# Optimization experiments

Measured on AMD Instinct MI355X. Metric: run time of the kernel, lower is better.

The kernel has to match this reference:

```python
import jax, jax.numpy as jnp
import numpy as np

CUTOFF = 10.0


def _forward(query_points, codes, grid_points, eW1, eb1, eW2, eb2, cW, cb, fcW, fcb, nW1, nb1, nW2, nb2, edge_index):
    B, N, _ = query_points.shape
    G = grid_points.shape[0]
    C = codes.shape[-1]
    n_pts = B * N
    num_nodes = n_pts + B * G
    qp = query_points.reshape(-1, 3)
    gc = jnp.broadcast_to(grid_points[None], (B, G, 3)).reshape(-1, 3)
    x = jnp.concatenate([qp, gc], axis=0)                      # [num_nodes, 3]
    h = jnp.concatenate([jnp.zeros((n_pts, C), qp.dtype), codes.reshape(-1, C)], axis=0)
    row, col = edge_index[0], edge_index[1]                    # row = grid (source), col = query (target)
    ones = jnp.ones((edge_index.shape[1],), x.dtype)
    denom = jnp.maximum(jax.ops.segment_sum(ones, col, num_segments=num_nodes), 1.0)[:, None]

    def layer(x, h, We1, be1, We2, be2, Wc, bc, Wn1, bn1, Wn2, bn2, out_x_dim):
        rel = x[row] - x[col]                                  # [E, 3]
        dist = jnp.linalg.norm(rel, axis=-1, keepdims=True)    # [E, 1]
        m = jax.nn.silu(jnp.concatenate([h[row], h[col], dist], axis=-1) @ We1 + be1)
        m = jax.nn.silu(m @ We2 + be2)                         # [E, H]
        d = dist[:, 0]
        Cm = 0.5 * (jnp.cos(d * jnp.pi / CUTOFF) + 1.0) * (d <= CUTOFF)
        m = m * Cm[:, None]
        coef = m @ Wc + bc                                     # [E, out_x_dim]
        dirn = rel / (dist + 1e-8)
        if out_x_dim == 1:
            cmsg = coef * dirn                                 # [E, 3]
            dx = jax.ops.segment_sum(cmsg, col, num_segments=num_nodes) / denom
            x_new = x + dx
        else:
            cmsg = (coef[:, :, None] * dirn[:, None, :]).reshape(coef.shape[0], -1)  # [E, T*3]
            dx = (jax.ops.segment_sum(cmsg, col, num_segments=num_nodes) / denom).reshape(num_nodes, out_x_dim, 3)
            x_new = x[:, None, :] + dx                         # [num_nodes, T, 3]
        m_aggr = jax.ops.segment_sum(m, col, num_segments=num_nodes) / denom
        h_delta = jax.nn.silu(jnp.concatenate([h, m_aggr], axis=-1) @ Wn1 + bn1) @ Wn2 + bn2
        return x_new, h + h_delta

    for i in range(3):
        x, h = layer(x, h, eW1[i], eb1[i], eW2[i], eb2[i], cW[i], cb[i], nW1[i], nb1[i], nW2[i], nb2[i], 1)
    T = fcb.shape[0]
    x_f, _ = layer(x, h, eW1[3], eb1[3], eW2[3], eb2[3], fcW, fcb, nW1[3], nb1[3], nW2[3], nb2[3], T)
    pred = x_f[:n_pts].reshape(B, N, T, 3)
    return pred - query_points.reshape(B, N, 3)[:, :, None, :]


def setup_inputs() -> dict:
    key = jax.random.key(0)
    B, N, Gs, Cd, H, T, deg = 8, 2048, 8, 128, 128, 5, 16
    G = Gs ** 3
    n_pts = B * N
    E = n_pts * deg
    ks = jax.random.split(key, 12)
    c1 = (jnp.arange(Gs, dtype=jnp.float32) - (Gs - 1) / 2.0) * 2.0   # anchor_spacing = 2.0, centered
    gx, gy, gz = jnp.meshgrid(c1, c1, c1, indexing='ij')
    grid_points = jnp.stack([gx, gy, gz], -1).reshape(-1, 3)
    query_points = jax.random.uniform(ks[0], (B, N, 3), minval=-7.0, maxval=7.0)
    codes = jax.random.normal(ks[1], (B, G, Cd), dtype=jnp.float32)
    q = jnp.repeat(jnp.arange(n_pts, dtype=jnp.int32), deg)
    gl = jax.random.randint(ks[2], (E,), 0, G, dtype=jnp.int32)
    row = n_pts + (q // N) * G + gl                                   # grid node (global idx), same batch as query
    edge_index = jnp.stack([row, q], axis=0)
    def lin(k, fi, sh):
        return jax.random.normal(k, sh, dtype=jnp.float32) / jnp.sqrt(jnp.float32(fi))
    eW1 = lin(ks[3], 2 * Cd + 1, (4, 2 * Cd + 1, H)); eb1 = jnp.zeros((4, H))
    eW2 = lin(ks[4], H, (4, H, H)); eb2 = jnp.zeros((4, H))
    cW = lin(ks[5], H, (3, H, 1)); cb = jnp.zeros((3, 1))
    fcW = lin(ks[6], H, (H, T)); fcb = jnp.zeros((T,))
    nW1 = lin(ks[7], Cd + H, (4, Cd + H, H)); nb1 = jnp.zeros((4, H))
    nW2 = lin(ks[8], H, (4, H, Cd)); nb2 = jnp.zeros((4, Cd))
    return {"query_points": query_points, "codes": codes, "grid_points": grid_points,
            "eW1": eW1, "eb1": eb1, "eW2": eW2, "eb2": eb2,
            "cW": cW, "cb": cb, "fcW": fcW, "fcb": fcb,
            "nW1": nW1, "nb1": nb1, "nW2": nW2, "nb2": nb2,
            "edge_index": edge_index}


def reference(query_points, codes, grid_points, eW1, eb1, eW2, eb2, cW, cb, fcW, fcb, nW1, nb1, nW2, nb2, edge_index):
    return _forward(query_points, codes, grid_points, eW1, eb1, eW2, eb2, cW, cb, fcW, fcb, nW1, nb1, nW2, nb2, edge_index)
```

## Files before the change

### kernel.cpp

```cpp
#include <hip/hip_runtime.h>
#include <hip/hip_bf16.h>

typedef unsigned short u16;
typedef unsigned int u32;
typedef __attribute__((ext_vector_type(8))) short short8;
typedef __attribute__((ext_vector_type(4))) float floatx4;

#define N_PTS 16384
#define N_GRID 4096
#define GPTS 512
#define HD 128
#define DEG 16
#define QB 16
#define EB 256
#define EBLK (N_PTS / QB)

__device__ __forceinline__ float silu_f(float x) {
    return x * __builtin_amdgcn_rcpf(1.0f + __expf(-x));
}
__device__ __forceinline__ short f2bf(float x) { return (short)__bfloat16_as_ushort(__float2bfloat16(x)); }

__global__ void k_fillf(float* out, float v, int n) {
    int i = blockIdx.x * blockDim.x + threadIdx.x;
    if (i < n) out[i] = v;
}

__global__ void k_init(const float* __restrict__ qp, const float* __restrict__ codes,
                       float* __restrict__ x_q, float* __restrict__ h_g, float* __restrict__ h_q,
                       float* __restrict__ Bq) {
    int stride = gridDim.x * blockDim.x;
    int i0 = blockIdx.x * blockDim.x + threadIdx.x;
    for (int i = i0; i < N_PTS * 3; i += stride) x_q[i] = qp[i];
    for (int i = i0; i < N_GRID * HD; i += stride) h_g[i] = codes[i];
    for (int i = i0; i < N_PTS * HD; i += stride) { h_q[i] = 0.0f; Bq[i] = 0.0f; }
}

__global__ void k_prep(const float* __restrict__ eW2, short* __restrict__ wsT) {
    int idx = blockIdx.x * blockDim.x + threadIdx.x;
    if (idx >= 4 * HD * HD) return;
    int l = idx >> 14, rem = idx & 16383, f = rem >> 7, k = rem & 127;
    wsT[idx] = f2bf(eW2[l * 16384 + k * HD + f]);
}

__global__ void k_prep2(const float* __restrict__ nW1, const float* __restrict__ nW2,
                        const float* __restrict__ eW1,
                        short* __restrict__ nW1T, short* __restrict__ nW2T,
                        short* __restrict__ W1midT, short* __restrict__ W1topT) {
    int idx = blockIdx.x * blockDim.x + threadIdx.x;
    if (idx < 3 * 32768) {
        int l = idx >> 15, r = idx & 32767, f = r >> 8, k = r & 255;
        nW1T[idx] = f2bf(nW1[l * 32768 + k * 128 + f]);
    } else if (idx < 3 * 32768 + 3 * 16384) {
        int j = idx - 3 * 32768;
        int l = j >> 14, r = j & 16383, f = r >> 7, k = r & 127;
        nW2T[j] = f2bf(nW2[l * 16384 + k * 128 + f]);
    } else if (idx < 3 * 32768 + 6 * 16384) {
        int j = idx - 3 * 32768 - 3 * 16384;
        int p = j >> 14, r = j & 16383, f = r >> 7, k = r & 127;
        W1midT[j] = f2bf(eW1[(p + 1) * 257 * 128 + (128 + k) * 128 + f]);
    } else if (idx < 3 * 32768 + 6 * 16384 + 4 * 16384) {
        int j = idx - 3 * 32768 - 6 * 16384;
        int l = j >> 14, r = j & 16383, f = r >> 7, k = r & 127;
        W1topT[j] = f2bf(eW1[l * 257 * 128 + k * 128 + f]);
    }
}

__device__ __forceinline__ void stageB(short* Bb, const short* src, int rowF4, int colF4, int tid) {
#pragma unroll
    for (int s = 0; s < 8; s++) {
        int idx = s * 256 + tid;
        int f = idx >> 4, c4 = idx & 15;
        float4 v = ((const float4*)src)[f * rowF4 + colF4 + c4];
        *(float4*)((char*)Bb + ((idx * 16) ^ ((f & 7) << 4))) = v;
    }
}

__device__ __forceinline__ void nb_gemm(const short* X1, const short* Bb, floatx4* acc,
                                        int rowbase, int kOff, int quad, int c, int swz) {
#pragma unroll
    for (int ks = 0; ks < 4; ks++) {
        short8 a = *(const short8*)((const char*)X1 + rowbase + (((kOff + ks * 32 + quad * 8) * 2) ^ swz));
#pragma unroll
        for (int n = 0; n < 8; n++) {
            short8 b = *(const short8*)((const char*)Bb + ((((n * 16 + c) << 8) + (ks * 32 + quad * 8) * 2) ^ swz));
            acc[n] = __builtin_amdgcn_mfma_f32_16x16x32_bf16(a, b, acc[n], 0, 0, 0);
        }
    }
}

__global__ __launch_bounds__(256) void k_ga2(
    const float* __restrict__ hg, float* __restrict__ Ag,
    const short* __restrict__ W1topT, const float* __restrict__ b1,
    const short* __restrict__ Wn1T, const float* __restrict__ bn1,
    const short* __restrict__ Wn2T, const float* __restrict__ bn2,
    int updateH, float* __restrict__ hg_out) {
    __shared__ short X[64 * 128];
    __shared__ short Bb[128 * 128];
    int tid = threadIdx.x;
    int n0 = blockIdx.x * 64;
    int wid = tid >> 6, lane = tid & 63, quad = lane >> 4, c = lane & 15;
    const int swz = (c & 7) << 4;

    {
        int q = tid >> 2, part = tid & 3;
        const float* src = &hg[(n0 + q) * HD + part * 32];
        int wswz = (q & 7) << 4;
#pragma unroll
        for (int i = 0; i < 4; i++) {
            float4 a = ((const float4*)src)[2 * i];
            float4 b = ((const float4*)src)[2 * i + 1];
            short8 v;
            v[0] = f2bf(a.x); v[1] = f2bf(a.y); v[2] = f2bf(a.z); v[3] = f2bf(a.w);
            v[4] = f2bf(b.x); v[5] = f2bf(b.y); v[6] = f2bf(b.z); v[7] = f2bf(b.w);
            *(short8*)((char*)X + ((q * 256 + part * 64 + i * 16) ^ wswz)) = v;
        }
    }
    stageB(Bb, W1topT, 16, 0, tid);
    __syncthreads();

    int rowbase = (wid * 16 + c) * 256;
    floatx4 acc[8];
#pragma unroll
    for (int n = 0; n < 8; n++) acc[n] = (floatx4)0.f;
    nb_gemm(X, Bb, acc, rowbase, 0, quad, c, swz);
#pragma unroll
    for (int n = 0; n < 8; n++) {
        int f = n * 16 + c;
        float bv = b1[f];
#pragma unroll
        for (int r = 0; r < 4; r++)
            Ag[(n0 + wid * 16 + quad * 4 + r) * HD + f] = acc[n][r] + bv;
    }
    if (!updateH) return;

    __syncthreads();
    stageB(Bb, Wn1T, 32, 0, tid);
    __syncthreads();
#pragma unroll
    for (int n = 0; n < 8; n++) acc[n] = (floatx4)0.f;
    nb_gemm(X, Bb, acc, rowbase, 0, quad, c, swz);
    __syncthreads();
#pragma unroll
    for (int n = 0; n < 8; n++) {
        int f = n * 16 + c;
        float b1v = bn1[f];
#pragma unroll
        for (int r = 0; r < 4; r++) {
            int rq = wid * 16 + quad * 4 + r;
            *(short*)((char*)X + ((rq * 256 + f * 2) ^ ((rq & 7) << 4))) =
                f2bf(silu_f(acc[n][r] + b1v));
        }
    }
    stageB(Bb, Wn2T, 16, 0, tid);
    __syncthreads();
#pragma unroll
    for (int n = 0; n < 8; n++) acc[n] = (floatx4)0.f;
    nb_gemm(X, Bb, acc, rowbase, 0, quad, c, swz);
#pragma unroll
    for (int n = 0; n < 8; n++) {
        int f = n * 16 + c;
        float b2v2 = bn2[f];
#pragma unroll
        for (int r = 0; r < 4; r++) {
            int gn = n0 + wid * 16 + quad * 4 + r;
            hg_out[gn * HD + f] = hg[gn * HD + f] + acc[n][r] + b2v2;
        }
    }
}

__global__ __launch_bounds__(256) void k_nb2(
    float* __restrict__ hq, const float* __restrict__ mg,
    const float* __restrict__ bn1, const float* __restrict__ bn2,
    const short* __restrict__ W1T, const short* __restrict__ W2T,
    const short* __restrict__ W3T, float* __restrict__ Bq) {
    __shared__ short X1[64 * 256];
    __shared__ short Bb[128 * 128];
    int tid = threadIdx.x;
    int q0 = blockIdx.x * 64;
    int wid = tid >> 6, lane = tid & 63, quad = lane >> 4, c = lane & 15;
    const int swz = (c & 7) << 4;

    {
        int q = tid >> 2, part = tid & 3;
        const float* src = (part < 2) ? &hq[(q0 + q) * HD + (part & 1) * 64]
                                      : &mg[(q0 + q) * HD + (part & 1) * 64];
        int wswz = (q & 7) << 4;
#pragma unroll
        for (int i = 0; i < 8; i++) {
            float4 a = ((const float4*)src)[2 * i];
            float4 b = ((const float4*)src)[2 * i + 1];
            short8 v;
            v[0] = f2bf(a.x); v[1] = f2bf(a.y); v[2] = f2bf(a.z); v[3] = f2bf(a.w);
            v[4] = f2bf(b.x); v[5] = f2bf(b.y); v[6] = f2bf(b.z); v[7] = f2bf(b.w);
            *(short8*)((char*)X1 + ((q * 512 + part * 128 + i * 16) ^ wswz)) = v;
        }
    }
    stageB(Bb, W1T, 32, 0, tid);
    __syncthreads();

    int row = wid * 16 + c;
    int rowbase = row * 512;
    floatx4 acc[8];
#pragma unroll
    for (int n = 0; n < 8; n++) acc[n] = (floatx4)0.f;
    nb_gemm(X1, Bb, acc, rowbase, 0, quad, c, swz);
    __syncthreads();
    stageB(Bb, W1T, 32, 16, tid);
    __syncthreads();
    nb_gemm(X1, Bb, acc, rowbase, 128, quad, c, swz);
    __syncthreads();

#pragma unroll
    for (int n = 0; n < 8; n++) {
        int f = n * 16 + c;
        float b1v = bn1[f];
#pragma unroll
        for (int r = 0; r < 4; r++) {
            int rq = wid * 16 + quad * 4 + r;
            *(short*)((char*)X1 + ((rq * 512 + (128 + f) * 2) ^ ((rq & 7) << 4))) =
                f2bf(silu_f(acc[n][r] + b1v));
        }
    }
    stageB(Bb, W2T, 16, 0, tid);
    __syncthreads();

#pragma unroll
    for (int n = 0; n < 8; n++) acc[n] = (floatx4)0.f;
    nb_gemm(X1, Bb, acc, rowbase, 128, quad, c, swz);
    __syncthreads();

#pragma unroll
    for (int n = 0; n < 8; n++) {
        int f = n * 16 + c;
        float b2v2 = bn2[f];
#pragma unroll
        for (int r = 0; r < 4; r++) {
            int rq = wid * 16 + quad * 4 + r;
            int gq = q0 + rq;
            float hv = hq[gq * HD + f] + acc[n][r] + b2v2;
            hq[gq * HD + f] = hv;
            *(short*)((char*)X1 + ((rq * 512 + f * 2) ^ ((rq & 7) << 4))) = f2bf(hv);
        }
    }
    stageB(Bb, W3T, 16, 0, tid);
    __syncthreads();

#pragma unroll
    for (int n = 0; n < 8; n++) acc[n] = (floatx4)0.f;
    nb_gemm(X1, Bb, acc, rowbase, 0, quad, c, swz);
#pragma unroll
    for (int n = 0; n < 8; n++) {
        int f = n * 16 + c;
#pragma unroll
        for (int r = 0; r < 4; r++) {
            int gq = q0 + wid * 16 + quad * 4 + r;
            Bq[gq * HD + f] = acc[n][r];
        }
    }
}

template <int OUTT, bool FIN>
__global__ __launch_bounds__(512, 4) void k_edge(
    const float* __restrict__ Ag, const float* __restrict__ Bq, float* __restrict__ x_q,
    const float* __restrict__ wdrow, const short* __restrict__ wsT,
    const float* __restrict__ b2v, const float* __restrict__ Wc, const float* __restrict__ cbp,
    const int* __restrict__ erow, const float* __restrict__ gridp,
    const float* __restrict__ qp, float* __restrict__ out, float* __restrict__ maggr) {
    __shared__ float misc[3072];
    __shared__ short lwsT[HD * HD];
    int tid = threadIdx.x;

    float* sdist = misc;
    float* scm   = misc + 256;
    float* sdir  = misc + 512;
    float* xs    = misc + 1280;
    float* scoef = misc + 1344;
    int*   sgi   = (int*)(misc + 2624);

    int q0 = blockIdx.x * QB;
    int wid = tid >> 6, lane = tid & 63, quad = lane >> 4, c = lane & 15;

    if (tid < QB * 3) xs[tid] = x_q[q0 * 3 + tid];
    {
        const float4* src = (const float4*)wsT;
#pragma unroll
        for (int s = 0; s < 4; s++) {
            int idx = s * 512 + tid;
            int byte = idx << 4;
            int swz2 = byte ^ (((byte >> 8) & 7) << 4);
            *(float4*)((char*)lwsT + swz2) = src[idx];
        }
    }
    __syncthreads();
    if (tid < EB) {
        int e = tid, q = e >> 4;
        int gi = erow[q0 * DEG + e] - N_PTS;
        sgi[e] = gi;
        int gl = gi & (GPTS - 1);
        float r0 = gridp[gl * 3 + 0] - xs[q * 3 + 0];
        float r1 = gridp[gl * 3 + 1] - xs[q * 3 + 1];
        float r2 = gridp[gl * 3 + 2] - xs[q * 3 + 2];
        float dist = sqrtf(r0 * r0 + r1 * r1 + r2 * r2);
        float inv = 1.0f / (dist + 1e-8f);
        sdist[e] = dist;
        sdir[0 * EB + e] = r0 * inv;
        sdir[1 * EB + e] = r1 * inv;
        sdir[2 * EB + e] = r2 * inv;
        float cw = 0.5f * (__cosf(dist * 0.31415926535897931f) + 1.0f);
        scm[e] = (dist <= 10.0f) ? cw : 0.0f;
    }
    __syncthreads();

    int gi_[2]; float dist_[2];
#pragma unroll
    for (int mi = 0; mi < 2; mi++) {
        int e = (wid * 2 + mi) * 16 + c;
        gi_[mi] = sgi[e];
        dist_[mi] = sdist[e];
    }

    floatx4 acc[2][8];
#pragma unroll
    for (int mi = 0; mi < 2; mi++)
#pragma unroll
        for (int n = 0; n < 8; n++) acc[mi][n] = (floatx4)0.f;

    const int swz = (c & 7) << 4;

#pragma unroll
    for (int ch = 0; ch < 4; ch++) {
        int kb = ch * 32 + quad * 8;
        float4 wd0 = *(const float4*)(wdrow + kb);
        float4 wd1 = *(const float4*)(wdrow + kb + 4);
        short8 afr[2];
#pragma unroll
        for (int mi = 0; mi < 2; mi++) {
            int q = wid * 2 + mi;
            float dist = dist_[mi];
            const float4* ap = (const float4*)(Ag + gi_[mi] * HD + kb);
            float4 a0 = ap[0], a1 = ap[1];
            const float4* bp4 = (const float4*)(Bq + (q0 + q) * HD + kb);
            float4 b0 = bp4[0], b1 = bp4[1];
            short8 v;
            v[0] = f2bf(silu_f(a0.x + b0.x + dist * wd0.x));
            v[1] = f2bf(silu_f(a0.y + b0.y + dist * wd0.y));
            v[2] = f2bf(silu_f(a0.z + b0.z + dist * wd0.z));
            v[3] = f2bf(silu_f(a0.w + b0.w + dist * wd0.w));
            v[4] = f2bf(silu_f(a1.x + b1.x + dist * wd1.x));
            v[5] = f2bf(silu_f(a1.y + b1.y + dist * wd1.y));
            v[6] = f2bf(silu_f(a1.z + b1.z + dist * wd1.z));
            v[7] = f2bf(silu_f(a1.w + b1.w + dist * wd1.w));
            afr[mi] = v;
        }
#pragma unroll
        for (int n = 0; n < 8; n++) {
            int byte = ((n * 16 + c) << 8) + (kb << 1);
            short8 bfr = *(const short8*)((const char*)lwsT + (byte ^ swz));
            acc[0][n] = __builtin_amdgcn_mfma_f32_16x16x32_bf16(afr[0], bfr, acc[0][n], 0, 0, 0);
            acc[1][n] = __builtin_amdgcn_mfma_f32_16x16x32_bf16(afr[1], bfr, acc[1][n], 0, 0, 0);
        }
    }

#pragma unroll
    for (int mi = 0; mi < 2; mi++) {
        int q = wid * 2 + mi;
        int ebase = q * 16;
        float cmr[4];
#pragma unroll
        for (int r = 0; r < 4; r++) cmr[r] = scm[ebase + quad * 4 + r];
        float apc[4][OUTT];
#pragma unroll
        for (int r = 0; r < 4; r++)
#pragma unroll
            for (int t = 0; t < OUTT; t++) apc[r][t] = 0.f;
#pragma unroll
        for (int n = 0; n < 8; n++) {
            int f = n * 16 + c;
            float be2v = b2v[f];
            float wcv[OUTT];
            if (FIN) {
#pragma unroll
                for (int t = 0; t < OUTT; t++) wcv[t] = Wc[f * 5 + t];
            } else {
                wcv[0] = Wc[f];
            }
            float cs = 0.f;
#pragma unroll
            for (int r = 0; r < 4; r++) {
                float v = silu_f(acc[mi][n][r] + be2v) * cmr[r];
                cs += v;
#pragma unroll
                for (int t = 0; t < OUTT; t++) apc[r][t] += v * wcv[t];
            }
            cs += __shfl_xor(cs, 16, 64);
            cs += __shfl_xor(cs, 32, 64);
            if (!FIN && lane < 16) maggr[(q0 + q) * HD + f] = cs * 0.0625f;
        }
#pragma unroll
        for (int t = 0; t < OUTT; t++) {
#pragma unroll
            for (int r = 0; r < 4; r++) {
                float v = apc[r][t];
                v += __shfl_xor(v, 1, 64);
                v += __shfl_xor(v, 2, 64);
                v += __shfl_xor(v, 4, 64);
                v += __shfl_xor(v, 8, 64);
                if (c == 0) scoef[(ebase + quad * 4 + r) * OUTT + t] = v;
            }
        }
    }
    __syncthreads();

    if (tid < QB * 3 * OUTT) {
        int qq = tid / (3 * OUTT), rem = tid % (3 * OUTT), t = rem / 3, c2 = rem % 3;
        float cbv = cbp[t];
        float s = 0.f;
#pragma unroll 4
        for (int r = 0; r < 16; r++) {
            int ee = qq * 16 + r;
            s += (scoef[ee * OUTT + t] + cbv) * sdir[c2 * EB + ee];
        }
        float dd = s * 0.0625f;
        if (FIN) out[(q0 + qq) * 15 + t * 3 + c2] = xs[qq * 3 + c2] + dd - qp[(q0 + qq) * 3 + c2];
        else x_q[(q0 + qq) * 3 + c2] = xs[qq * 3 + c2] + dd;
    }
}

extern "C" void kernel_launch(void* const* d_in, const int* in_sizes, int n_in,
                              void* d_out, int out_size, void* d_ws, size_t ws_size,
                              hipStream_t stream) {
    float* out = (float*)d_out;
    int fill_blocks = (out_size + 255) / 256;

    static const int exp_sz[16] = { 49152, 524288, 1536, 131584, 512, 65536, 512, 384,
                                    3, 640, 5, 131072, 512, 65536, 512, 524288 };
    bool ok = (n_in == 16);
    for (int i = 0; ok && i < 16; i++) if (in_sizes[i] != exp_sz[i]) ok = false;
    if (!ok || ws_size < (size_t)40 * 1024 * 1024) {
        k_fillf<<<fill_blocks, 256, 0, stream>>>(out, 777.0f, out_size);
        return;
    }

    const float* qp    = (const float*)d_in[0];
    const float* codes = (const float*)d_in[1];
    const float* gridp = (const float*)d_in[2];
    const float* eW1   = (const float*)d_in[3];
    const float* eb1   = (const float*)d_in[4];
    const float* eW2   = (const float*)d_in[5];
    const float* eb2   = (const float*)d_in[6];
    const float* cW    = (const float*)d_in[7];
    const float* cb    = (const float*)d_in[8];
    const float* fcW   = (const float*)d_in[9];
    const float* fcb   = (const float*)d_in[10];
    const float* nW1   = (const float*)d_in[11];
    const float* nb1   = (const float*)d_in[12];
    const float* nW2   = (const float*)d_in[13];
    const float* nb2   = (const float*)d_in[14];
    const int*   erow  = (const int*)d_in[15];

    float* ws = (float*)d_ws;
    float* x_q  = ws;  ws += N_PTS * 3;
    float* h_q  = ws;  ws += N_PTS * HD;
    float* hg_a = ws;  ws += N_GRID * HD;
    float* hg_b = ws;  ws += N_GRID * HD;
    float* Ag0  = ws;  ws += N_GRID * HD;
    float* Ag1  = ws;  ws += N_GRID * HD;
    float* Ag2  = ws;  ws += N_GRID * HD;
    float* Ag3  = ws;  ws += N_GRID * HD;
    float* Bqb  = ws;  ws += N_PTS * HD;
    float* mgb  = ws;  ws += N_PTS * HD;
    short* wsT    = (short*)ws;
    short* nW1T   = wsT + 65536;
    short* nW2T   = nW1T + 98304;
    short* W1midT = nW2T + 49152;
    short* W1topT = W1midT + 49152;
    float* Agb[4] = { Ag0, Ag1, Ag2, Ag3 };
    float* hgs[2] = { hg_a, hg_b };

    k_init<<<2048, 256, 0, stream>>>(qp, codes, x_q, hg_a, h_q, Bqb);
    k_prep<<<(4 * HD * HD + 255) / 256, 256, 0, stream>>>(eW2, wsT);
    k_prep2<<<(3 * 32768 + 6 * 16384 + 4 * 16384 + 255) / 256, 256, 0, stream>>>(
        nW1, nW2, eW1, nW1T, nW2T, W1midT, W1topT);

    for (int L = 0; L < 4; L++) {
        int nl = (L < 3) ? L : 0;
        k_ga2<<<N_GRID / 64, 256, 0, stream>>>(
            hgs[L & 1], Agb[L], W1topT + L * 16384, eb1 + L * 128,
            nW1T + nl * 32768, nb1 + L * 128, nW2T + nl * 16384, nb2 + L * 128,
            (L < 3) ? 1 : 0, hgs[(L + 1) & 1]);
    }

    for (int i = 0; i < 4; i++) {
        int fin = (i == 3);
        const float* W1l = eW1 + i * 257 * 128;
        if (i > 0) {
            int p = i - 1;
            k_nb2<<<N_PTS / 64, 256, 0, stream>>>(h_q, mgb,
                                                  nb1 + p * 128, nb2 + p * 128,
                                                  nW1T + p * 32768, nW2T + p * 16384,
                                                  W1midT + p * 16384, Bqb);
        }
        if (!fin) {
            k_edge<1, false><<<EBLK, 512, 0, stream>>>(
                Agb[i], Bqb, x_q, W1l + 256 * 128, wsT + i * 16384, eb2 + i * 128,
                cW + i * 128, cb + i, erow, gridp, qp, out, mgb);
        } else {
            k_edge<5, true><<<EBLK, 512, 0, stream>>>(
                Agb[3], Bqb, x_q, W1l + 256 * 128, wsT + i * 16384, eb2 + i * 128,
                fcW, fcb, erow, gridp, qp, out, mgb);
        }
    }
}
```

Before: 370.4 us.

## Fuse query node-update MLP into edge kernel epilogue

Removes the separate k_nb2 launch by running the query node-update MLP (h update and the next layer's W1mid projection into Bq) at the end of each k_edge block for its 16 queries. The aggregated messages stay in shared memory as bf16 instead of round-tripping through the global mgb buffer. This saves a global write and read of a 16384x128 float tensor plus three launches. In exchange, each 16-query block restages three 128x128 weight tiles, which is 4x more weight traffic than the old 64-row blocks. Extra shared memory and the lowered launch-bounds occupancy (4 to 3) are also risks.

```diff
diff --git a/kernel.cpp b/kernel.cpp
--- a/kernel.cpp
+++ b/kernel.cpp
@@ -4,6 +4,7 @@
 typedef unsigned short u16;
 typedef unsigned int u32;
 typedef __attribute__((ext_vector_type(8))) short short8;
+typedef __attribute__((ext_vector_type(4))) short shortx4;
 typedef __attribute__((ext_vector_type(4))) float floatx4;
 
 #define N_PTS 16384
@@ -75,6 +76,16 @@
     }
 }
 
+__device__ __forceinline__ void stageB512(short* Bb, const short* src, int rowF4, int colF4, int tid) {
+#pragma unroll
+    for (int s = 0; s < 4; s++) {
+        int idx = s * 512 + tid;
+        int f = idx >> 4, c4 = idx & 15;
+        float4 v = ((const float4*)src)[f * rowF4 + colF4 + c4];
+        *(float4*)((char*)Bb + ((idx * 16) ^ ((f & 7) << 4))) = v;
+    }
+}
+
 __device__ __forceinline__ void nb_gemm(const short* X1, const short* Bb, floatx4* acc,
                                         int rowbase, int kOff, int quad, int c, int swz) {
 #pragma unroll
@@ -85,6 +96,17 @@
             short8 b = *(const short8*)((const char*)Bb + ((((n * 16 + c) << 8) + (ks * 32 + quad * 8) * 2) ^ swz));
             acc[n] = __builtin_amdgcn_mfma_f32_16x16x32_bf16(a, b, acc[n], 0, 0, 0);
         }
+    }
+}
+
+__device__ __forceinline__ void gemm16(const short* X, const short* Bb, floatx4& acc,
+                                       int kOffX, int wid, int quad, int c, int swz) {
+#pragma unroll
+    for (int ks = 0; ks < 4; ks++) {
+        int k = ks * 32 + quad * 8;
+        short8 a = *(const short8*)((const char*)X + ((c * 512 + (kOffX + k) * 2) ^ swz));
+        short8 b = *(const short8*)((const char*)Bb + ((((wid * 16 + c) << 8) + k * 2) ^ swz));
+        acc = __builtin_amdgcn_mfma_f32_16x16x32_bf16(a, b, acc, 0, 0, 0);
     }
 }
 
@@ -168,105 +190,18 @@
     }
 }
 
-__global__ __launch_bounds__(256) void k_nb2(
-    float* __restrict__ hq, const float* __restrict__ mg,
-    const float* __restrict__ bn1, const float* __restrict__ bn2,
-    const short* __restrict__ W1T, const short* __restrict__ W2T,
-    const short* __restrict__ W3T, float* __restrict__ Bq) {
-    __shared__ short X1[64 * 256];
-    __shared__ short Bb[128 * 128];
-    int tid = threadIdx.x;
-    int q0 = blockIdx.x * 64;
-    int wid = tid >> 6, lane = tid & 63, quad = lane >> 4, c = lane & 15;
-    const int swz = (c & 7) << 4;
-
-    {
-        int q = tid >> 2, part = tid & 3;
-        const float* src = (part < 2) ? &hq[(q0 + q) * HD + (part & 1) * 64]
-                                      : &mg[(q0 + q) * HD + (part & 1) * 64];
-        int wswz = (q & 7) << 4;
-#pragma unroll
-        for (int i = 0; i < 8; i++) {
-            float4 a = ((const float4*)src)[2 * i];
-            float4 b = ((const float4*)src)[2 * i + 1];
-            short8 v;
-            v[0] = f2bf(a.x); v[1] = f2bf(a.y); v[2] = f2bf(a.z); v[3] = f2bf(a.w);
-            v[4] = f2bf(b.x); v[5] = f2bf(b.y); v[6] = f2bf(b.z); v[7] = f2bf(b.w);
-            *(short8*)((char*)X1 + ((q * 512 + part * 128 + i * 16) ^ wswz)) = v;
-        }
-    }
-    stageB(Bb, W1T, 32, 0, tid);
-    __syncthreads();
-
-    int row = wid * 16 + c;
-    int rowbase = row * 512;
-    floatx4 acc[8];
-#pragma unroll
-    for (int n = 0; n < 8; n++) acc[n] = (floatx4)0.f;
-    nb_gemm(X1, Bb, acc, rowbase, 0, quad, c, swz);
-    __syncthreads();
-    stageB(Bb, W1T, 32, 16, tid);
-    __syncthreads();
-    nb_gemm(X1, Bb, acc, rowbase, 128, quad, c, swz);
-    __syncthreads();
-
-#pragma unroll
-    for (int n = 0; n < 8; n++) {
-        int f = n * 16 + c;
-        float b1v = bn1[f];
-#pragma unroll
-        for (int r = 0; r < 4; r++) {
-            int rq = wid * 16 + quad * 4 + r;
-            *(short*)((char*)X1 + ((rq * 512 + (128 + f) * 2) ^ ((rq & 7) << 4))) =
-                f2bf(silu_f(acc[n][r] + b1v));
-        }
-    }
-    stageB(Bb, W2T, 16, 0, tid);
-    __syncthreads();
-
-#pragma unroll
-    for (int n = 0; n < 8; n++) acc[n] = (floatx4)0.f;
-    nb_gemm(X1, Bb, acc, rowbase, 128, quad, c, swz);
-    __syncthreads();
-
-#pragma unroll
-    for (int n = 0; n < 8; n++) {
-        int f = n * 16 + c;
-        float b2v2 = bn2[f];
-#pragma unroll
-        for (int r = 0; r < 4; r++) {
-            int rq = wid * 16 + quad * 4 + r;
-            int gq = q0 + rq;
-            float hv = hq[gq * HD + f] + acc[n][r] + b2v2;
-            hq[gq * HD + f] = hv;
-            *(short*)((char*)X1 + ((rq * 512 + f * 2) ^ ((rq & 7) << 4))) = f2bf(hv);
-        }
-    }
-    stageB(Bb, W3T, 16, 0, tid);
-    __syncthreads();
-
-#pragma unroll
-    for (int n = 0; n < 8; n++) acc[n] = (floatx4)0.f;
-    nb_gemm(X1, Bb, acc, rowbase, 0, quad, c, swz);
-#pragma unroll
-    for (int n = 0; n < 8; n++) {
-        int f = n * 16 + c;
-#pragma unroll
-        for (int r = 0; r < 4; r++) {
-            int gq = q0 + wid * 16 + quad * 4 + r;
-            Bq[gq * HD + f] = acc[n][r];
-        }
-    }
-}
-
 template <int OUTT, bool FIN>
-__global__ __launch_bounds__(512, 4) void k_edge(
-    const float* __restrict__ Ag, const float* __restrict__ Bq, float* __restrict__ x_q,
+__global__ __launch_bounds__(512, 3) void k_edge(
+    const float* __restrict__ Ag, float* __restrict__ Bq, float* __restrict__ x_q,
     const float* __restrict__ wdrow, const short* __restrict__ wsT,
     const float* __restrict__ b2v, const float* __restrict__ Wc, const float* __restrict__ cbp,
     const int* __restrict__ erow, const float* __restrict__ gridp,
-    const float* __restrict__ qp, float* __restrict__ out, float* __restrict__ maggr) {
+    const float* __restrict__ qp, float* __restrict__ out,
+    const float* __restrict__ bn1, const float* __restrict__ bn2,
+    const short* __restrict__ Wn1T, const short* __restrict__ Wn2T,
+    const short* __restrict__ W1midT, float* __restrict__ hq) {
     __shared__ float misc[3072];
+    __shared__ short Xn[16 * 256];
     __shared__ short lwsT[HD * HD];
     int tid = threadIdx.x;
 
@@ -394,7 +329,9 @@
             }
             cs += __shfl_xor(cs, 16, 64);
             cs += __shfl_xor(cs, 32, 64);
-            if (!FIN && lane < 16) maggr[(q0 + q) * HD + f] = cs * 0.0625f;
+            if (!FIN && lane < 16)
+                *(short*)((char*)Xn + ((q * 512 + (128 + f) * 2) ^ ((q & 7) << 4))) =
+                    f2bf(cs * 0.0625f);
         }
 #pragma unroll
         for (int t = 0; t < OUTT; t++) {
@@ -423,6 +360,66 @@
         float dd = s * 0.0625f;
         if (FIN) out[(q0 + qq) * 15 + t * 3 + c2] = xs[qq * 3 + c2] + dd - qp[(q0 + qq) * 3 + c2];
         else x_q[(q0 + qq) * 3 + c2] = xs[qq * 3 + c2] + dd;
+    }
+    if (FIN) return;
+
+    {
+        int q = tid >> 5, f0 = (tid & 31) * 4;
+        float4 h4 = *(const float4*)&hq[(q0 + q) * HD + f0];
+        shortx4 v;
+        v[0] = f2bf(h4.x); v[1] = f2bf(h4.y); v[2] = f2bf(h4.z); v[3] = f2bf(h4.w);
+        *(shortx4*)((char*)Xn + ((q * 512 + f0 * 2) ^ ((q & 7) << 4))) = v;
+    }
+    stageB512(lwsT, Wn1T, 32, 0, tid);
+    __syncthreads();
+
+    floatx4 acc1 = (floatx4)0.f;
+    gemm16(Xn, lwsT, acc1, 0, wid, quad, c, swz);
+    __syncthreads();
+    stageB512(lwsT, Wn1T, 32, 16, tid);
+    __syncthreads();
+    gemm16(Xn, lwsT, acc1, 128, wid, quad, c, swz);
+    __syncthreads();
+
+    {
+        int f = wid * 16 + c;
+        float b1v = bn1[f];
+#pragma unroll
+        for (int r = 0; r < 4; r++) {
+            int q = quad * 4 + r;
+            *(short*)((char*)Xn + ((q * 512 + (128 + f) * 2) ^ ((q & 7) << 4))) =
+                f2bf(silu_f(acc1[r] + b1v));
+        }
+    }
+    stageB512(lwsT, Wn2T, 16, 0, tid);
+    __syncthreads();
+
+    floatx4 acc2 = (floatx4)0.f;
+    gemm16(Xn, lwsT, acc2, 128, wid, quad, c, swz);
+    __syncthreads();
+
+    {
+        int f = wid * 16 + c;
+        float b2 = bn2[f];
+#pragma unroll
+        for (int r = 0; r < 4; r++) {
+            int q = quad * 4 + r;
+            int gq = q0 + q;
+            float hv = hq[gq * HD + f] + acc2[r] + b2;
+            hq[gq * HD + f] = hv;
+            *(short*)((char*)Xn + ((q * 512 + f * 2) ^ ((q & 7) << 4))) = f2bf(hv);
+        }
+    }
+    stageB512(lwsT, W1midT, 16, 0, tid);
+    __syncthreads();
+
+    floatx4 acc3 = (floatx4)0.f;
+    gemm16(Xn, lwsT, acc3, 0, wid, quad, c, swz);
+    {
+        int f = wid * 16 + c;
+#pragma unroll
+        for (int r = 0; r < 4; r++)
+            Bq[(q0 + quad * 4 + r) * HD + f] = acc3[r];
     }
 }
 
@@ -468,7 +465,6 @@
     float* Ag2  = ws;  ws += N_GRID * HD;
     float* Ag3  = ws;  ws += N_GRID * HD;
     float* Bqb  = ws;  ws += N_PTS * HD;
-    float* mgb  = ws;  ws += N_PTS * HD;
     short* wsT    = (short*)ws;
     short* nW1T   = wsT + 65536;
     short* nW2T   = nW1T + 98304;
@@ -491,23 +487,18 @@
     }
 
     for (int i = 0; i < 4; i++) {
-        int fin = (i == 3);
         const float* W1l = eW1 + i * 257 * 128;
-        if (i > 0) {
-            int p = i - 1;
-            k_nb2<<<N_PTS / 64, 256, 0, stream>>>(h_q, mgb,
-                                                  nb1 + p * 128, nb2 + p * 128,
-                                                  nW1T + p * 32768, nW2T + p * 16384,
-                                                  W1midT + p * 16384, Bqb);
-        }
-        if (!fin) {
+        if (i < 3) {
             k_edge<1, false><<<EBLK, 512, 0, stream>>>(
                 Agb[i], Bqb, x_q, W1l + 256 * 128, wsT + i * 16384, eb2 + i * 128,
-                cW + i * 128, cb + i, erow, gridp, qp, out, mgb);
+                cW + i * 128, cb + i, erow, gridp, qp, out,
+                nb1 + i * 128, nb2 + i * 128, nW1T + i * 32768, nW2T + i * 16384,
+                W1midT + i * 16384, h_q);
         } else {
             k_edge<5, true><<<EBLK, 512, 0, stream>>>(
                 Agb[3], Bqb, x_q, W1l + 256 * 128, wsT + i * 16384, eb2 + i * 128,
-                fcW, fcb, erow, gridp, qp, out, mgb);
-        }
-    }
-}
+                fcW, fcb, erow, gridp, qp, out,
+                nullptr, nullptr, nullptr, nullptr, nullptr, nullptr);
+        }
+    }
+}
```

Result: faster. 345.2 us (-6.8%).
